# Performance work log

Hardware: AMD Instinct MI355X
Metric: run time of the kernel (lower is better)

The kernel has to match this reference:

```python
import jax, jax.numpy as jnp
import numpy as np

B, T, N, K, C = 4, 12, 2000, 8, 32
AGG_N = 4  # mean, max, min, std
EPS = 1e-5


def sparsify(a, k):
    # keep top-k entries per row, zero the rest (torch.topk + torch.where)
    thr = jax.lax.top_k(a, k)[0][..., -1:]
    return jnp.where(a < thr, jnp.zeros_like(a), a)


def aggregate(I, adj):
    # I: (b,t,n,f), adj: (b,n,n) row-sparsified with K nonzeros per row
    deg = jnp.sum(adj, axis=-1)[:, None, :, None]              # (b,1,n,1)
    mean = jnp.einsum('bnm,btmf->btnf', adj, I) / deg
    meansq = jnp.einsum('bnm,btmf->btnf', adj, I * I) / deg
    std = jnp.sqrt(jax.nn.relu(meansq - mean * mean) + EPS)
    vals, idx = jax.lax.top_k(adj, K)                          # (b,n,K)
    nb = jax.vmap(lambda Ib, ib: Ib[:, ib])(I, idx)            # (b,t,n,K,f)
    valid = (vals > 0)[:, None, :, :, None]
    mx = jnp.max(jnp.where(valid, nb, -jnp.inf), axis=3)
    mn = jnp.min(jnp.where(valid, nb, jnp.inf), axis=3)
    return jnp.concatenate([mean, mx, mn, std], axis=3)


def stower(x, adj, Theta, bias, masking, use_scalers):
    # x: (b,c,t,n) -> out: (b,o,t,n)
    I = jnp.transpose(x, (0, 2, 3, 1))                          # (b,t,n,c)
    m = aggregate(I, adj)
    if masking:
        m = jnp.where(jnp.isnan(m), 6.0, m)
        m = jnp.where(jnp.isinf(m), 0.0, m)
        m = jnp.minimum(m, 6.0)
    if use_scalers:
        deg = jnp.sum((adj > 0).astype(m.dtype), axis=-1)       # (b,n)
        s = jnp.log1p(deg)[:, None, :, None]
        m = jnp.concatenate([m, m * s, m / s], axis=3)
    out = jnp.einsum('btji,io->btjo', m, Theta) + bias
    return jnp.transpose(out, (0, 3, 1, 2))


def tcn(x, W, b):
    # tcn_layer2 with act='linear': tanh(conv1x1(x) + x)
    return jnp.tanh(jnp.einsum('oc,bctn->botn', W, x) + b[None, :, None, None] + x)


def setup_inputs():
    key = jax.random.key(0)
    ks = jax.random.split(key, 14)
    stdv = 1.0 / np.sqrt(C)
    u = lambda k, shape: jax.random.uniform(k, shape, jnp.float32, -stdv, stdv)
    return {
        'X': jax.random.normal(ks[0], (B, T, N, 1), jnp.float32),
        'adj': jax.random.uniform(ks[1], (N, N), jnp.float32),
        'adj_mask': jax.random.uniform(ks[2], (N, N), jnp.float32),
        'Theta0': u(ks[3], (AGG_N * 1, C)),   # len(agg)*len(['identity'])*in_variables
        'bias0': u(ks[4], (C,)),
        'Wt0': u(ks[5], (C, C)),
        'bt0': u(ks[6], (C,)),
        'Theta1': u(ks[7], (AGG_N * 3 * C, C)),  # len(agg)*len(scalers)*channels
        'bias1': u(ks[8], (C,)),
        'Wt1': u(ks[9], (C, C)),
        'bt1': u(ks[10], (C,)),
        'Wout': u(ks[11], (1, C)),
        'bout': u(ks[12], (1,)),
        'batch_seen': 0,
        'epoch': 0,
        'train': 0,
    }


def reference(X, adj, adj_mask, Theta0, bias0, Wt0, bt0, Theta1, bias1, Wt1, bt1, Wout, bout, batch_seen, epoch, train):
    x0 = X[:, None, :, :, 0]                                   # (b,1,t,n)
    adj_s = sparsify(jnp.broadcast_to(adj, (B, N, N)), K)
    adjm_s = sparsify(jnp.broadcast_to(adj_mask, (B, N, N)), K)
    h = stower(x0, adjm_s, Theta0, bias0, True, False)         # s_layer0 (masking, identity scaler)
    h = tcn(h, Wt0, bt0)                                       # t_layer0
    h = jax.nn.relu(stower(h, adj_s, Theta1, bias1, False, True))
    h = jax.nn.relu(tcn(h, Wt1, bt1))
    y = jnp.einsum('oc,bctn->botn', Wout, h) + bout[None, :, None, None]
    return y.reshape(B, T, N)
```

## Files before the change

kernel.cpp:

```cpp
#include <hip/hip_runtime.h>
#include <hip/hip_bf16.h>
#include <math.h>

#define BB 4
#define TT 12
#define NN 2000
#define KK 8
#define CC 32
#define EPSF 1e-5f
#define LISTCAP 16
#define NSITES (BB * TT * NN)
#define MACRO 64
#define NMACRO (NSITES / MACRO)

typedef __bf16 bf16x8 __attribute__((ext_vector_type(8)));
typedef float  f32x4  __attribute__((ext_vector_type(4)));

__device__ __forceinline__ unsigned short f2bf(float x) {
    union { __hip_bfloat16 h; unsigned short u; } c;
    c.h = __float2bfloat16(x);
    return c.u;
}
__device__ __forceinline__ float bf2f(unsigned short u) {
    return __uint_as_float(((unsigned)u) << 16);
}

__device__ __forceinline__ float mask6(float v) {
    if (isnan(v)) v = 6.0f;
    if (isinf(v)) v = 0.0f;
    return fminf(v, 6.0f);
}

__device__ __forceinline__ unsigned long long shflx64(unsigned long long v, int m) {
    int lo = __shfl_xor((int)(unsigned)(v & 0xffffffffull), m, 64);
    int hi = __shfl_xor((int)(unsigned)(v >> 32), m, 64);
    return ((unsigned long long)(unsigned)hi << 32) | (unsigned)lo;
}

__global__ __launch_bounds__(256)
void topk_prep(const float* __restrict__ adj, const float* __restrict__ adjm,
               int* __restrict__ t_idx, float* __restrict__ t_val,
               int* __restrict__ t_cnt, int* __restrict__ t_scnt,
               float* __restrict__ t_deg)
{
    __shared__ int wext[4][8];
    __shared__ int wextn[4];
    const int tid = threadIdx.x;
    const int wid = tid >> 6, lane = tid & 63;
    if (lane == 0) wextn[wid] = 0;

    const int grow = blockIdx.x * 4 + wid;
    const int mat = (grow >= NN) ? 1 : 0;
    const int row = grow - mat * NN;
    const float* src = (mat == 0 ? adjm : adj) + (size_t)row * NN;

    unsigned long long key[8];
    #pragma unroll
    for (int j = 0; j < 8; ++j) key[j] = 0ull;

    for (int i = lane; i < NN; i += 64) {
        float v = src[i];
        unsigned long long nk =
            ((unsigned long long)__float_as_uint(v) << 32) | (unsigned)(~(unsigned)i);
        if (nk > key[7]) {
            #pragma unroll
            for (int j = 7; j >= 1; --j)
                key[j] = (nk > key[j - 1]) ? key[j - 1] : ((nk > key[j]) ? nk : key[j]);
            if (nk > key[0]) key[0] = nk;
        }
    }

    #pragma unroll
    for (int d = 1; d < 64; d <<= 1) {
        unsigned long long ok[8], c[8];
        #pragma unroll
        for (int j = 0; j < 8; ++j) ok[j] = shflx64(key[j], d);
        #pragma unroll
        for (int j = 0; j < 8; ++j) {
            unsigned long long o = ok[7 - j];
            c[j] = (key[j] > o) ? key[j] : o;
        }
        #pragma unroll
        for (int st = 4; st >= 1; st >>= 1) {
            #pragma unroll
            for (int j = 0; j < 8; ++j) {
                if ((j & st) == 0 && (j | st) < 8) {
                    unsigned long long a = c[j], b = c[j | st];
                    unsigned long long hi = (a > b) ? a : b;
                    unsigned long long lo = (a > b) ? b : a;
                    c[j] = hi; c[j | st] = lo;
                }
            }
        }
        #pragma unroll
        for (int j = 0; j < 8; ++j) key[j] = c[j];
    }

    const float thr = __uint_as_float((unsigned)(key[7] >> 32));

    float degp = 0.f; int cp = 0;
    for (int i = lane; i < NN; i += 64) {
        float v = src[i];
        if (v >= thr) {
            degp += v;
            if (v > 0.f) cp++;
            if (v == thr) {
                unsigned long long nk =
                    ((unsigned long long)__float_as_uint(v) << 32) | (unsigned)(~(unsigned)i);
                if (nk < key[7]) {
                    int p = atomicAdd(&wextn[wid], 1);
                    if (p < 8) wext[wid][p] = i;
                }
            }
        }
    }
    #pragma unroll
    for (int off = 32; off >= 1; off >>= 1) {
        degp += __shfl_xor(degp, off, 64);
        cp   += __shfl_xor(cp, off, 64);
    }
    __syncthreads();

    if (lane == 0) {
        int en = wextn[wid]; if (en > 8) en = 8;
        const size_t ob = (size_t)grow * LISTCAP;
        #pragma unroll
        for (int j = 0; j < 8; ++j) {
            t_idx[ob + j] = (int)(~(unsigned)(key[j] & 0xffffffffull));
            t_val[ob + j] = __uint_as_float((unsigned)(key[j] >> 32));
        }
        for (int j = 0; j < 8; ++j) {
            t_idx[ob + 8 + j] = (j < en) ? wext[wid][j] : 0;
            t_val[ob + 8 + j] = (j < en) ? thr : 0.f;
        }
        t_cnt[grow]  = 8 + en;
        t_scnt[grow] = cp;
        t_deg[grow]  = degp;
    }
}

__global__ __launch_bounds__(256)
void stower0_tcn0(const float* __restrict__ X,
                  const int* __restrict__ t_idx, const float* __restrict__ t_val,
                  const int* __restrict__ t_cnt, const float* __restrict__ t_deg,
                  const float* __restrict__ Theta0, const float* __restrict__ bias0,
                  const float* __restrict__ Wt0, const float* __restrict__ bt0,
                  float* __restrict__ I1)
{
    const int site = blockIdx.x * 256 + threadIdx.x;
    const int n  = site % NN;
    const int bt = site / NN;
    const float* xrow = X + (size_t)bt * NN;

    const size_t base = (size_t)n * LISTCAP;
    const int cnt   = t_cnt[n];
    const float deg = t_deg[n];
    float wsum = 0.f, wsq = 0.f, mx = -INFINITY, mn = INFINITY;
    for (int j = 0; j < cnt; ++j) {
        int   id = t_idx[base + j];
        float w  = t_val[base + j];
        float xv = xrow[id];
        wsum = fmaf(w, xv, wsum);
        wsq  = fmaf(w * xv, xv, wsq);
        if (j < KK && w > 0.f) { mx = fmaxf(mx, xv); mn = fminf(mn, xv); }
    }
    float mean = wsum / deg;
    float var  = wsq / deg - mean * mean;
    float sd   = sqrtf(fmaxf(var, 0.f) + EPSF);
    float m0 = mask6(mean), m1 = mask6(mx), m2 = mask6(mn), m3 = mask6(sd);

    float h0[CC];
    #pragma unroll
    for (int c = 0; c < CC; ++c) {
        float v = bias0[c];
        v = fmaf(m0, Theta0[0 * CC + c], v);
        v = fmaf(m1, Theta0[1 * CC + c], v);
        v = fmaf(m2, Theta0[2 * CC + c], v);
        v = fmaf(m3, Theta0[3 * CC + c], v);
        h0[c] = v;
    }
    float* op = I1 + (size_t)site * CC;
    #pragma unroll
    for (int c = 0; c < CC; ++c) {
        float acc = bt0[c] + h0[c];
        #pragma unroll
        for (int k = 0; k < CC; ++k) acc = fmaf(Wt0[c * CC + k], h0[k], acc);
        op[c] = tanhf(acc);
    }
}

__global__ __launch_bounds__(256, 2)
void stower1_tcn1_out(const float* __restrict__ I1,
                      const int* __restrict__ t_idx, const float* __restrict__ t_val,
                      const int* __restrict__ t_cnt, const int* __restrict__ t_scnt,
                      const float* __restrict__ t_deg,
                      const float* __restrict__ Theta1, const float* __restrict__ bias1,
                      const float* __restrict__ Wt1, const float* __restrict__ bt1,
                      const float* __restrict__ Wout, const float* __restrict__ bout,
                      float* __restrict__ out)
{
    __shared__ unsigned short sBhi[96 * 128];
    __shared__ unsigned short sBlo[96 * 128];
    __shared__ unsigned short sAhi[64 * 128];
    __shared__ unsigned short sAlo[64 * 128];
    float* h_t = reinterpret_cast<float*>(sAhi);

    const int tid = threadIdx.x;

    for (int i = tid; i < 384 * 32; i += 256) {
        const int row = i >> 5;
        const int o   = i & 31;
        const int jm  = row >> 7;
        const int k   = row & 127;
        const int nt  = jm * 2 + (o >> 4);
        const int n   = o & 15;
        const float v = Theta1[i];
        const unsigned short hi = f2bf(v);
        const unsigned short lo = f2bf(v - bf2f(hi));
        const int idx = (nt * 16 + n) * 128 + (((k >> 3) ^ n) << 3) + (k & 7);
        sBhi[idx] = hi; sBlo[idx] = lo;
    }

    const int lane = tid & 63;
    const int w    = tid >> 6;
    const int m15  = lane & 15;
    const int q    = lane >> 4;
    const int sl   = tid >> 5;
    const int f    = tid & 31;

    float wrow[CC];
    #pragma unroll
    for (int c = 0; c < CC; ++c) wrow[c] = Wt1[f * CC + c];
    const float bt1f  = bt1[f];
    const float woutf = Wout[f];
    const float boutv = bout[0];
    const float b1a = bias1[m15];
    const float b1b = bias1[16 + m15];
    __syncthreads();

    for (int mb = blockIdx.x; mb < NMACRO; mb += gridDim.x) {
        const int sbase = mb * MACRO;

        #pragma unroll 1
        for (int it = 0; it < 8; ++it) {
            const int s = it * 8 + sl;
            const int site = sbase + s;
            const int n  = site % NN;
            const int bt = site / NN;
            const size_t rbase = (size_t)(NN + n) * LISTCAP;
            const int cnt   = t_cnt[NN + n];
            const float deg = t_deg[NN + n];
            const float* Ibt = I1 + (size_t)bt * NN * CC;

            const int4   i0 = *(const int4*)&t_idx[rbase];
            const int4   i1 = *(const int4*)&t_idx[rbase + 4];
            const float4 w0 = *(const float4*)&t_val[rbase];
            const float4 w1 = *(const float4*)&t_val[rbase + 4];

            float x0 = Ibt[(size_t)i0.x * CC + f];
            float x1 = Ibt[(size_t)i0.y * CC + f];
            float x2 = Ibt[(size_t)i0.z * CC + f];
            float x3 = Ibt[(size_t)i0.w * CC + f];
            float x4 = Ibt[(size_t)i1.x * CC + f];
            float x5 = Ibt[(size_t)i1.y * CC + f];
            float x6 = Ibt[(size_t)i1.z * CC + f];
            float x7 = Ibt[(size_t)i1.w * CC + f];

            float wsum = 0.f, wsq = 0.f, mx = -INFINITY, mn = INFINITY;
            #define AGG(wv, xv) do { \
                wsum = fmaf(wv, xv, wsum); wsq = fmaf(wv * xv, xv, wsq); \
                if (wv > 0.f) { mx = fmaxf(mx, xv); mn = fminf(mn, xv); } } while (0)
            AGG(w0.x, x0); AGG(w0.y, x1); AGG(w0.z, x2); AGG(w0.w, x3);
            AGG(w1.x, x4); AGG(w1.y, x5); AGG(w1.z, x6); AGG(w1.w, x7);
            #undef AGG
            if (cnt > 8) {
                for (int j = 8; j < cnt; ++j) {
                    int   id = t_idx[rbase + j];
                    float wv = t_val[rbase + j];
                    float xv = Ibt[(size_t)id * CC + f];
                    wsum = fmaf(wv, xv, wsum);
                    wsq  = fmaf(wv * xv, xv, wsq);
                }
            }
            float mean = wsum / deg;
            float var  = wsq / deg - mean * mean;
            float sd   = sqrtf(fmaxf(var, 0.f) + EPSF);

            const int sx = s & 15;
            const int b  = s * 128;
            const int fh = f >> 3, fl = f & 7;
            const int ia = b + (((0 + fh) ^ sx) << 3) + fl;
            const int ib = b + (((4 + fh) ^ sx) << 3) + fl;
            const int ic = b + (((8 + fh) ^ sx) << 3) + fl;
            const int id_ = b + (((12 + fh) ^ sx) << 3) + fl;
            unsigned short h0 = f2bf(mean); sAhi[ia] = h0; sAlo[ia] = f2bf(mean - bf2f(h0));
            unsigned short h1 = f2bf(mx);   sAhi[ib] = h1; sAlo[ib] = f2bf(mx   - bf2f(h1));
            unsigned short h2 = f2bf(mn);   sAhi[ic] = h2; sAlo[ic] = f2bf(mn   - bf2f(h2));
            unsigned short h3 = f2bf(sd);   sAhi[id_] = h3; sAlo[id_] = f2bf(sd  - bf2f(h3));
        }
        __syncthreads();

        f32x4 acc[6];
        #pragma unroll
        for (int t = 0; t < 6; ++t) acc[t] = (f32x4){0.f, 0.f, 0.f, 0.f};

        const int arow = (w * 16 + m15) * 128;
        #pragma unroll
        for (int ks = 0; ks < 4; ++ks) {
            const int kb   = ks * 4 + q;
            const int koff = ((kb ^ m15) << 3);
            const bf16x8 ah = *reinterpret_cast<const bf16x8*>(&sAhi[arow + koff]);
            const bf16x8 al = *reinterpret_cast<const bf16x8*>(&sAlo[arow + koff]);
            #pragma unroll
            for (int t = 0; t < 6; ++t) {
                const int bidx = (t * 16 + m15) * 128 + koff;
                const bf16x8 bh = *reinterpret_cast<const bf16x8*>(&sBhi[bidx]);
                const bf16x8 bl = *reinterpret_cast<const bf16x8*>(&sBlo[bidx]);
                acc[t] = __builtin_amdgcn_mfma_f32_16x16x32_bf16(ah, bh, acc[t], 0, 0, 0);
                acc[t] = __builtin_amdgcn_mfma_f32_16x16x32_bf16(ah, bl, acc[t], 0, 0, 0);
                acc[t] = __builtin_amdgcn_mfma_f32_16x16x32_bf16(al, bh, acc[t], 0, 0, 0);
            }
        }
        __syncthreads();

        #pragma unroll
        for (int r = 0; r < 4; ++r) {
            const int sloc = q * 4 + r;
            const int site = sbase + w * 16 + sloc;
            const int n    = site % NN;
            const float s1  = log1pf((float)t_scnt[NN + n]);
            const float is1 = 1.0f / s1;
            float ha = acc[0][r] + s1 * acc[2][r] + is1 * acc[4][r] + b1a;
            float hb = acc[1][r] + s1 * acc[3][r] + is1 * acc[5][r] + b1b;
            ha = fmaxf(ha, 0.f); hb = fmaxf(hb, 0.f);
            h_t[(w * 16 + sloc) * 36 + m15]      = ha;
            h_t[(w * 16 + sloc) * 36 + 16 + m15] = hb;
        }
        __syncthreads();

        #pragma unroll 1
        for (int j = 0; j < 8; ++j) {
            const int s = sl * 8 + j;
            const float* hp = &h_t[s * 36];
            float acc3 = bt1f + hp[f];
            #pragma unroll
            for (int qq = 0; qq < 8; ++qq) {
                float4 h4 = *(const float4*)&hp[qq * 4];
                acc3 = fmaf(wrow[qq * 4 + 0], h4.x, acc3);
                acc3 = fmaf(wrow[qq * 4 + 1], h4.y, acc3);
                acc3 = fmaf(wrow[qq * 4 + 2], h4.z, acc3);
                acc3 = fmaf(wrow[qq * 4 + 3], h4.w, acc3);
            }
            float y = fmaxf(tanhf(acc3), 0.f) * woutf;
            #pragma unroll
            for (int off = 16; off >= 1; off >>= 1)
                y += __shfl_xor(y, off, 64);
            if (f == 0) out[sbase + s] = y + boutv;
        }
        __syncthreads();
    }
}

extern "C" void kernel_launch(void* const* d_in, const int* in_sizes, int n_in,
                              void* d_out, int out_size, void* d_ws, size_t ws_size,
                              hipStream_t stream)
{
    const float* X      = (const float*)d_in[0];
    const float* adj    = (const float*)d_in[1];
    const float* adjm   = (const float*)d_in[2];
    const float* Theta0 = (const float*)d_in[3];
    const float* bias0  = (const float*)d_in[4];
    const float* Wt0    = (const float*)d_in[5];
    const float* bt0    = (const float*)d_in[6];
    const float* Theta1 = (const float*)d_in[7];
    const float* bias1  = (const float*)d_in[8];
    const float* Wt1    = (const float*)d_in[9];
    const float* bt1    = (const float*)d_in[10];
    const float* Wout   = (const float*)d_in[11];
    const float* bout   = (const float*)d_in[12];
    (void)in_sizes; (void)n_in; (void)out_size; (void)ws_size;

    char* p = (char*)d_ws;
    int*   t_idx  = (int*)p;   p += (size_t)2 * NN * LISTCAP * sizeof(int);
    float* t_val  = (float*)p; p += (size_t)2 * NN * LISTCAP * sizeof(float);
    int*   t_cnt  = (int*)p;   p += (size_t)2 * NN * sizeof(int);
    int*   t_scnt = (int*)p;   p += (size_t)2 * NN * sizeof(int);
    float* t_deg  = (float*)p; p += (size_t)2 * NN * sizeof(float);
    float* I1     = (float*)p; p += (size_t)NSITES * CC * sizeof(float);

    hipLaunchKernelGGL(topk_prep, dim3(2 * NN / 4), dim3(256), 0, stream,
                       adj, adjm, t_idx, t_val, t_cnt, t_scnt, t_deg);
    hipLaunchKernelGGL(stower0_tcn0, dim3(NSITES / 256), dim3(256), 0, stream,
                       X, t_idx, t_val, t_cnt, t_deg, Theta0, bias0, Wt0, bt0, I1);
    hipLaunchKernelGGL(stower1_tcn1_out, dim3(500), dim3(256), 0, stream,
                       I1, t_idx, t_val, t_cnt, t_scnt, t_deg,
                       Theta1, bias1, Wt1, bt1, Wout, bout, (float*)d_out);
}
```

Measured before the change: 211.3 us.

## Restructure final fused kernel: smaller macro tiles, MFMA for tcn1, register-held Theta1 hi

```diff
diff --git a/kernel.cpp b/kernel.cpp
--- a/kernel.cpp
+++ b/kernel.cpp
@@ -10,27 +10,29 @@
 #define EPSF 1e-5f
 #define LISTCAP 16
 #define NSITES (BB * TT * NN)
-#define MACRO 64
+#define MACRO 32
 #define NMACRO (NSITES / MACRO)
-
+#define GRID_C 1000
+
+typedef unsigned short u16;
 typedef __bf16 bf16x8 __attribute__((ext_vector_type(8)));
 typedef float  f32x4  __attribute__((ext_vector_type(4)));
 
-__device__ __forceinline__ unsigned short f2bf(float x) {
-    union { __hip_bfloat16 h; unsigned short u; } c;
+union bfpack { bf16x8 v; u16 u[8]; };
+
+__device__ __forceinline__ u16 f2bf(float x) {
+    union { __hip_bfloat16 h; u16 u; } c;
     c.h = __float2bfloat16(x);
     return c.u;
 }
-__device__ __forceinline__ float bf2f(unsigned short u) {
+__device__ __forceinline__ float bf2f(u16 u) {
     return __uint_as_float(((unsigned)u) << 16);
 }
-
 __device__ __forceinline__ float mask6(float v) {
     if (isnan(v)) v = 6.0f;
     if (isinf(v)) v = 0.0f;
     return fminf(v, 6.0f);
 }
-
 __device__ __forceinline__ unsigned long long shflx64(unsigned long long v, int m) {
     int lo = __shfl_xor((int)(unsigned)(v & 0xffffffffull), m, 64);
     int hi = __shfl_xor((int)(unsigned)(v >> 32), m, 64);
@@ -40,8 +42,8 @@
 __global__ __launch_bounds__(256)
 void topk_prep(const float* __restrict__ adj, const float* __restrict__ adjm,
                int* __restrict__ t_idx, float* __restrict__ t_val,
-               int* __restrict__ t_cnt, int* __restrict__ t_scnt,
-               float* __restrict__ t_deg)
+               int* __restrict__ t_cnt, float* __restrict__ t_deg,
+               float* __restrict__ t_ideg, float2* __restrict__ t_sc)
 {
     __shared__ int wext[4][8];
     __shared__ int wextn[4];
@@ -134,8 +136,10 @@
             t_val[ob + 8 + j] = (j < en) ? thr : 0.f;
         }
         t_cnt[grow]  = 8 + en;
-        t_scnt[grow] = cp;
         t_deg[grow]  = degp;
+        t_ideg[grow] = 1.0f / degp;
+        float s1 = log1pf((float)cp);
+        t_sc[grow]   = make_float2(s1, 1.0f / s1);
     }
 }
 
@@ -189,67 +193,94 @@
     }
 }
 
-__global__ __launch_bounds__(256, 2)
+__global__ __launch_bounds__(256, 3)
 void stower1_tcn1_out(const float* __restrict__ I1,
                       const int* __restrict__ t_idx, const float* __restrict__ t_val,
-                      const int* __restrict__ t_cnt, const int* __restrict__ t_scnt,
-                      const float* __restrict__ t_deg,
+                      const int* __restrict__ t_cnt, const float* __restrict__ t_ideg,
+                      const float2* __restrict__ t_sc,
                       const float* __restrict__ Theta1, const float* __restrict__ bias1,
                       const float* __restrict__ Wt1, const float* __restrict__ bt1,
                       const float* __restrict__ Wout, const float* __restrict__ bout,
                       float* __restrict__ out)
 {
-    __shared__ unsigned short sBhi[96 * 128];
-    __shared__ unsigned short sBlo[96 * 128];
-    __shared__ unsigned short sAhi[64 * 128];
-    __shared__ unsigned short sAlo[64 * 128];
-    float* h_t = reinterpret_cast<float*>(sAhi);
-
-    const int tid = threadIdx.x;
-
-    for (int i = tid; i < 384 * 32; i += 256) {
-        const int row = i >> 5;
-        const int o   = i & 31;
-        const int jm  = row >> 7;
-        const int k   = row & 127;
-        const int nt  = jm * 2 + (o >> 4);
-        const int n   = o & 15;
-        const float v = Theta1[i];
-        const unsigned short hi = f2bf(v);
-        const unsigned short lo = f2bf(v - bf2f(hi));
-        const int idx = (nt * 16 + n) * 128 + (((k >> 3) ^ n) << 3) + (k & 7);
-        sBhi[idx] = hi; sBlo[idx] = lo;
-    }
-
+    __shared__ u16 sBlo[96 * 128];
+    __shared__ alignas(16) char uSpace[24576];
+    __shared__ float sPart[64];
+
+    u16*   stage = (u16*)uSpace;
+    u16*   sAhi  = (u16*)uSpace;
+    u16*   sAlo  = sAhi + 32 * 128;
+    u16*   hHi   = (u16*)uSpace;
+    u16*   hLo   = hHi + 32 * 40;
+    float* h32   = (float*)(uSpace + 5120);
+
+    const int tid  = threadIdx.x;
     const int lane = tid & 63;
     const int w    = tid >> 6;
     const int m15  = lane & 15;
     const int q    = lane >> 4;
     const int sl   = tid >> 5;
     const int f    = tid & 31;
-
-    float wrow[CC];
-    #pragma unroll
-    for (int c = 0; c < CC; ++c) wrow[c] = Wt1[f * CC + c];
-    const float bt1f  = bt1[f];
-    const float woutf = Wout[f];
+    const int hf   = w & 1;
+    const int st   = w >> 1;
+    const int ot   = w >> 1;
+    const int st2  = w & 1;
+
+    for (int i = tid; i < 384 * 32; i += 256) {
+        const int row = i >> 5, o = i & 31;
+        const int jm = row >> 7, k = row & 127;
+        const int nt = jm * 2 + (o >> 4), n = o & 15;
+        stage[(nt * 16 + n) * 128 + (((k >> 3) ^ n) << 3) + (k & 7)] = f2bf(Theta1[i]);
+    }
+    __syncthreads();
+    bf16x8 bH[3][4];
+    #pragma unroll
+    for (int j3 = 0; j3 < 3; ++j3) {
+        const int tile = 2 * j3 + hf;
+        #pragma unroll
+        for (int ks = 0; ks < 4; ++ks)
+            bH[j3][ks] = *(const bf16x8*)&stage[(tile * 16 + m15) * 128 +
+                                                (((ks * 4 + q) ^ m15) << 3)];
+    }
+    __syncthreads();
+    for (int i = tid; i < 384 * 32; i += 256) {
+        const int row = i >> 5, o = i & 31;
+        const int jm = row >> 7, k = row & 127;
+        const int nt = jm * 2 + (o >> 4), n = o & 15;
+        const float v = Theta1[i];
+        const u16 hi = f2bf(v);
+        sBlo[(nt * 16 + n) * 128 + (((k >> 3) ^ n) << 3) + (k & 7)] = f2bf(v - bf2f(hi));
+    }
+    bfpack bwh, bwl;
+    {
+        const float* wp = &Wt1[(ot * 16 + m15) * CC + q * 8];
+        const float4 v0 = *(const float4*)wp;
+        const float4 v1 = *(const float4*)(wp + 4);
+        const float vv[8] = {v0.x, v0.y, v0.z, v0.w, v1.x, v1.y, v1.z, v1.w};
+        #pragma unroll
+        for (int j = 0; j < 8; ++j) {
+            const u16 hi = f2bf(vv[j]);
+            bwh.u[j] = hi;
+            bwl.u[j] = f2bf(vv[j] - bf2f(hi));
+        }
+    }
+    const float b1o   = bias1[hf * 16 + m15];
+    const float bt1o  = bt1[ot * 16 + m15];
+    const float wouto = Wout[ot * 16 + m15];
     const float boutv = bout[0];
-    const float b1a = bias1[m15];
-    const float b1b = bias1[16 + m15];
-    __syncthreads();
-
-    for (int mb = blockIdx.x; mb < NMACRO; mb += gridDim.x) {
+
+    for (int mb = blockIdx.x; mb < NMACRO; mb += GRID_C) {
         const int sbase = mb * MACRO;
 
-        #pragma unroll 1
-        for (int it = 0; it < 8; ++it) {
+        #pragma unroll
+        for (int it = 0; it < 4; ++it) {
             const int s = it * 8 + sl;
             const int site = sbase + s;
             const int n  = site % NN;
             const int bt = site / NN;
             const size_t rbase = (size_t)(NN + n) * LISTCAP;
-            const int cnt   = t_cnt[NN + n];
-            const float deg = t_deg[NN + n];
+            const int cnt    = t_cnt[NN + n];
+            const float ideg = t_ideg[NN + n];
             const float* Ibt = I1 + (size_t)bt * NN * CC;
 
             const int4   i0 = *(const int4*)&t_idx[rbase];
@@ -257,19 +288,19 @@
             const float4 w0 = *(const float4*)&t_val[rbase];
             const float4 w1 = *(const float4*)&t_val[rbase + 4];
 
-            float x0 = Ibt[(size_t)i0.x * CC + f];
-            float x1 = Ibt[(size_t)i0.y * CC + f];
-            float x2 = Ibt[(size_t)i0.z * CC + f];
-            float x3 = Ibt[(size_t)i0.w * CC + f];
-            float x4 = Ibt[(size_t)i1.x * CC + f];
-            float x5 = Ibt[(size_t)i1.y * CC + f];
-            float x6 = Ibt[(size_t)i1.z * CC + f];
-            float x7 = Ibt[(size_t)i1.w * CC + f];
+            const float x0 = Ibt[(size_t)i0.x * CC + f];
+            const float x1 = Ibt[(size_t)i0.y * CC + f];
+            const float x2 = Ibt[(size_t)i0.z * CC + f];
+            const float x3 = Ibt[(size_t)i0.w * CC + f];
+            const float x4 = Ibt[(size_t)i1.x * CC + f];
+            const float x5 = Ibt[(size_t)i1.y * CC + f];
+            const float x6 = Ibt[(size_t)i1.z * CC + f];
+            const float x7 = Ibt[(size_t)i1.w * CC + f];
 
             float wsum = 0.f, wsq = 0.f, mx = -INFINITY, mn = INFINITY;
             #define AGG(wv, xv) do { \
                 wsum = fmaf(wv, xv, wsum); wsq = fmaf(wv * xv, xv, wsq); \
-                if (wv > 0.f) { mx = fmaxf(mx, xv); mn = fminf(mn, xv); } } while (0)
+                mx = fmaxf(mx, xv); mn = fminf(mn, xv); } while (0)
             AGG(w0.x, x0); AGG(w0.y, x1); AGG(w0.z, x2); AGG(w0.w, x3);
             AGG(w1.x, x4); AGG(w1.y, x5); AGG(w1.z, x6); AGG(w1.w, x7);
             #undef AGG
@@ -282,82 +313,87 @@
                     wsq  = fmaf(wv * xv, xv, wsq);
                 }
             }
-            float mean = wsum / deg;
-            float var  = wsq / deg - mean * mean;
-            float sd   = sqrtf(fmaxf(var, 0.f) + EPSF);
+            const float mean = wsum * ideg;
+            const float var  = wsq * ideg - mean * mean;
+            const float sd   = sqrtf(fmaxf(var, 0.f) + EPSF);
 
             const int sx = s & 15;
             const int b  = s * 128;
             const int fh = f >> 3, fl = f & 7;
-            const int ia = b + (((0 + fh) ^ sx) << 3) + fl;
-            const int ib = b + (((4 + fh) ^ sx) << 3) + fl;
-            const int ic = b + (((8 + fh) ^ sx) << 3) + fl;
+            const int ia  = b + (((0  + fh) ^ sx) << 3) + fl;
+            const int ib  = b + (((4  + fh) ^ sx) << 3) + fl;
+            const int ic  = b + (((8  + fh) ^ sx) << 3) + fl;
             const int id_ = b + (((12 + fh) ^ sx) << 3) + fl;
-            unsigned short h0 = f2bf(mean); sAhi[ia] = h0; sAlo[ia] = f2bf(mean - bf2f(h0));
-            unsigned short h1 = f2bf(mx);   sAhi[ib] = h1; sAlo[ib] = f2bf(mx   - bf2f(h1));
-            unsigned short h2 = f2bf(mn);   sAhi[ic] = h2; sAlo[ic] = f2bf(mn   - bf2f(h2));
-            unsigned short h3 = f2bf(sd);   sAhi[id_] = h3; sAlo[id_] = f2bf(sd  - bf2f(h3));
+            u16 h0 = f2bf(mean); sAhi[ia]  = h0; sAlo[ia]  = f2bf(mean - bf2f(h0));
+            u16 h1 = f2bf(mx);   sAhi[ib]  = h1; sAlo[ib]  = f2bf(mx   - bf2f(h1));
+            u16 h2 = f2bf(mn);   sAhi[ic]  = h2; sAlo[ic]  = f2bf(mn   - bf2f(h2));
+            u16 h3 = f2bf(sd);   sAhi[id_] = h3; sAlo[id_] = f2bf(sd   - bf2f(h3));
         }
         __syncthreads();
 
-        f32x4 acc[6];
-        #pragma unroll
-        for (int t = 0; t < 6; ++t) acc[t] = (f32x4){0.f, 0.f, 0.f, 0.f};
-
-        const int arow = (w * 16 + m15) * 128;
+        f32x4 acc[3];
+        #pragma unroll
+        for (int j3 = 0; j3 < 3; ++j3) acc[j3] = (f32x4){0.f, 0.f, 0.f, 0.f};
+
+        const int arow = (st * 16 + m15) * 128;
         #pragma unroll
         for (int ks = 0; ks < 4; ++ks) {
-            const int kb   = ks * 4 + q;
-            const int koff = ((kb ^ m15) << 3);
-            const bf16x8 ah = *reinterpret_cast<const bf16x8*>(&sAhi[arow + koff]);
-            const bf16x8 al = *reinterpret_cast<const bf16x8*>(&sAlo[arow + koff]);
+            const int koff = (((ks * 4 + q) ^ m15) << 3);
+            const bf16x8 aH = *(const bf16x8*)&sAhi[arow + koff];
+            const bf16x8 aL = *(const bf16x8*)&sAlo[arow + koff];
             #pragma unroll
-            for (int t = 0; t < 6; ++t) {
-                const int bidx = (t * 16 + m15) * 128 + koff;
-                const bf16x8 bh = *reinterpret_cast<const bf16x8*>(&sBhi[bidx]);
-                const bf16x8 bl = *reinterpret_cast<const bf16x8*>(&sBlo[bidx]);
-                acc[t] = __builtin_amdgcn_mfma_f32_16x16x32_bf16(ah, bh, acc[t], 0, 0, 0);
-                acc[t] = __builtin_amdgcn_mfma_f32_16x16x32_bf16(ah, bl, acc[t], 0, 0, 0);
-                acc[t] = __builtin_amdgcn_mfma_f32_16x16x32_bf16(al, bh, acc[t], 0, 0, 0);
+            for (int j3 = 0; j3 < 3; ++j3) {
+                const bf16x8 bL = *(const bf16x8*)&sBlo[((2 * j3 + hf) * 16 + m15) * 128 + koff];
+                acc[j3] = __builtin_amdgcn_mfma_f32_16x16x32_bf16(aH, bH[j3][ks], acc[j3], 0, 0, 0);
+                acc[j3] = __builtin_amdgcn_mfma_f32_16x16x32_bf16(aH, bL,          acc[j3], 0, 0, 0);
+                acc[j3] = __builtin_amdgcn_mfma_f32_16x16x32_bf16(aL, bH[j3][ks], acc[j3], 0, 0, 0);
             }
         }
         __syncthreads();
 
         #pragma unroll
         for (int r = 0; r < 4; ++r) {
-            const int sloc = q * 4 + r;
-            const int site = sbase + w * 16 + sloc;
+            const int sl2  = st * 16 + q * 4 + r;
+            const int site = sbase + sl2;
             const int n    = site % NN;
-            const float s1  = log1pf((float)t_scnt[NN + n]);
-            const float is1 = 1.0f / s1;
-            float ha = acc[0][r] + s1 * acc[2][r] + is1 * acc[4][r] + b1a;
-            float hb = acc[1][r] + s1 * acc[3][r] + is1 * acc[5][r] + b1b;
-            ha = fmaxf(ha, 0.f); hb = fmaxf(hb, 0.f);
-            h_t[(w * 16 + sloc) * 36 + m15]      = ha;
-            h_t[(w * 16 + sloc) * 36 + 16 + m15] = hb;
+            const float2 sc = t_sc[NN + n];
+            float h = acc[0][r] + sc.x * acc[1][r] + sc.y * acc[2][r] + b1o;
+            h = fmaxf(h, 0.f);
+            const int o = hf * 16 + m15;
+            const u16 hi = f2bf(h);
+            hHi[sl2 * 40 + o] = hi;
+            hLo[sl2 * 40 + o] = f2bf(h - bf2f(hi));
+            h32[sl2 * 33 + o] = h;
         }
         __syncthreads();
 
-        #pragma unroll 1
-        for (int j = 0; j < 8; ++j) {
-            const int s = sl * 8 + j;
-            const float* hp = &h_t[s * 36];
-            float acc3 = bt1f + hp[f];
+        f32x4 c2 = (f32x4){0.f, 0.f, 0.f, 0.f};
+        {
+            const bf16x8 ahh = *(const bf16x8*)&hHi[(st2 * 16 + m15) * 40 + q * 8];
+            const bf16x8 ahl = *(const bf16x8*)&hLo[(st2 * 16 + m15) * 40 + q * 8];
+            c2 = __builtin_amdgcn_mfma_f32_16x16x32_bf16(ahh, bwh.v, c2, 0, 0, 0);
+            c2 = __builtin_amdgcn_mfma_f32_16x16x32_bf16(ahh, bwl.v, c2, 0, 0, 0);
+            c2 = __builtin_amdgcn_mfma_f32_16x16x32_bf16(ahl, bwh.v, c2, 0, 0, 0);
+        }
+        float p[4];
+        #pragma unroll
+        for (int r = 0; r < 4; ++r) {
+            const int sl2 = st2 * 16 + q * 4 + r;
+            const float hres = h32[sl2 * 33 + ot * 16 + m15];
+            float yv = tanhf(c2[r] + bt1o + hres);
+            yv = fmaxf(yv, 0.f);
+            p[r] = yv * wouto;
             #pragma unroll
-            for (int qq = 0; qq < 8; ++qq) {
-                float4 h4 = *(const float4*)&hp[qq * 4];
-                acc3 = fmaf(wrow[qq * 4 + 0], h4.x, acc3);
-                acc3 = fmaf(wrow[qq * 4 + 1], h4.y, acc3);
-                acc3 = fmaf(wrow[qq * 4 + 2], h4.z, acc3);
-                acc3 = fmaf(wrow[qq * 4 + 3], h4.w, acc3);
-            }
-            float y = fmaxf(tanhf(acc3), 0.f) * woutf;
-            #pragma unroll
-            for (int off = 16; off >= 1; off >>= 1)
-                y += __shfl_xor(y, off, 64);
-            if (f == 0) out[sbase + s] = y + boutv;
-        }
+            for (int mk = 1; mk <= 8; mk <<= 1)
+                p[r] += __shfl_xor(p[r], mk, 64);
+        }
+        float selv  = (m15 & 1) ? p[1] : p[0];
+        float selv2 = (m15 & 1) ? p[3] : p[2];
+        selv = (m15 & 2) ? selv2 : selv;
+        if (m15 < 4) sPart[ot * 32 + st2 * 16 + q * 4 + m15] = selv;
         __syncthreads();
+
+        if (tid < 32) out[sbase + tid] = sPart[tid] + sPart[32 + tid] + boutv;
     }
 }
 
@@ -381,18 +417,19 @@
     (void)in_sizes; (void)n_in; (void)out_size; (void)ws_size;
 
     char* p = (char*)d_ws;
-    int*   t_idx  = (int*)p;   p += (size_t)2 * NN * LISTCAP * sizeof(int);
-    float* t_val  = (float*)p; p += (size_t)2 * NN * LISTCAP * sizeof(float);
-    int*   t_cnt  = (int*)p;   p += (size_t)2 * NN * sizeof(int);
-    int*   t_scnt = (int*)p;   p += (size_t)2 * NN * sizeof(int);
-    float* t_deg  = (float*)p; p += (size_t)2 * NN * sizeof(float);
-    float* I1     = (float*)p; p += (size_t)NSITES * CC * sizeof(float);
+    int*    t_idx  = (int*)p;    p += (size_t)2 * NN * LISTCAP * sizeof(int);
+    float*  t_val  = (float*)p;  p += (size_t)2 * NN * LISTCAP * sizeof(float);
+    int*    t_cnt  = (int*)p;    p += (size_t)2 * NN * sizeof(int);
+    float*  t_deg  = (float*)p;  p += (size_t)2 * NN * sizeof(float);
+    float*  t_ideg = (float*)p;  p += (size_t)2 * NN * sizeof(float);
+    float2* t_sc   = (float2*)p; p += (size_t)2 * NN * sizeof(float2);
+    float*  I1     = (float*)p;  p += (size_t)NSITES * CC * sizeof(float);
 
     hipLaunchKernelGGL(topk_prep, dim3(2 * NN / 4), dim3(256), 0, stream,
-                       adj, adjm, t_idx, t_val, t_cnt, t_scnt, t_deg);
+                       adj, adjm, t_idx, t_val, t_cnt, t_deg, t_ideg, t_sc);
     hipLaunchKernelGGL(stower0_tcn0, dim3(NSITES / 256), dim3(256), 0, stream,
                        X, t_idx, t_val, t_cnt, t_deg, Theta0, bias0, Wt0, bt0, I1);
-    hipLaunchKernelGGL(stower1_tcn1_out, dim3(500), dim3(256), 0, stream,
-                       I1, t_idx, t_val, t_cnt, t_scnt, t_deg,
+    hipLaunchKernelGGL(stower1_tcn1_out, dim3(GRID_C), dim3(256), 0, stream,
+                       I1, t_idx, t_val, t_cnt, t_ideg, t_sc,
                        Theta1, bias1, Wt1, bt1, Wout, bout, (float*)d_out);
 }
```

New measurement: 200.0 us. 1.06x faster.
